# Kernel optimization log

Hardware: AMD Instinct MI355X
Metric: run time of the kernel (lower is better)

Reference implementation:

```python
import jax
import jax.numpy as jnp
from jax import lax
import numpy as np

IN_SCALE, IN_ZP = 0.01, 7
W_SCALE, W_ZP = 0.01, 3
B_SCALE = 0.0001
I32_MIN, I32_MAX = -(2.0**31), 2.0**31 - 1


def setup_inputs() -> dict:
    key = jax.random.key(0)
    k1, k2, k3 = jax.random.split(key, 3)
    # int8 quantized input activations and weights (torch passes torch.int8 tensors)
    inputVec = jax.random.randint(k1, (32, 128, 56, 56), -128, 128, dtype=jnp.int32).astype(jnp.int8)
    weight = jax.random.randint(k2, (256, 128, 3, 3), -128, 128, dtype=jnp.int32).astype(jnp.int8)
    bias = jax.random.normal(k3, (256,), dtype=jnp.float32)
    return {"inputVec": inputVec, "weight": weight, "bias": bias}


def reference(inputVec, weight, bias):
    # dequantize per-tensor: (q - zero_point) * scale
    x = (inputVec.astype(jnp.float32) - IN_ZP) * IN_SCALE   # [N, Cin, H, W]
    w = (weight.astype(jnp.float32) - W_ZP) * W_SCALE       # [Cout, Cin, kh, kw]
    # quantize bias to qint32 (round-half-even, clamp to int32 range) then dequantize
    b = jnp.clip(jnp.round(bias / B_SCALE), I32_MIN, I32_MAX) * B_SCALE  # [Cout]
    # conv2d: stride 1, no padding, dilation 1, groups 1
    out = lax.conv_general_dilated(
        x, w,
        window_strides=(1, 1),
        padding='VALID',
        dimension_numbers=('NCHW', 'OIHW', 'NCHW'),
    )  # [N, Cout, H-2, W-2]
    return out + b[None, :, None, None]
```

## Files before the change

kernel.cpp:

```cpp
#include <hip/hip_runtime.h>
#include <hip/hip_bf16.h>


#define N_B   32
#define C_IN  128
#define H_IN  56
#define W_IN  56
#define C_OUT 256
#define H_OUT 54
#define W_OUT 54
#define K_TOT 1152
#define NPX   (N_B * H_OUT * W_OUT)
#define PXROW (H_OUT * W_OUT)

using i32x4  = __attribute__((ext_vector_type(4))) int;

static __device__ __forceinline__ int dot4(int a, int b, int c) {
#if __has_builtin(__builtin_amdgcn_sdot4)
  return __builtin_amdgcn_sdot4(a, b, c, false);
#else
  signed char a0 = (signed char)a, a1 = (signed char)(a >> 8),
              a2 = (signed char)(a >> 16), a3 = (signed char)(a >> 24);
  signed char b0 = (signed char)b, b1 = (signed char)(b >> 8),
              b2 = (signed char)(b >> 16), b3 = (signed char)(b >> 24);
  return c + a0 * b0 + a1 * b1 + a2 * b2 + a3 * b3;
#endif
}

static __device__ __forceinline__ int pack4(int4 v) {
  return (v.x & 255) | ((v.y & 255) << 8) | ((v.z & 255) << 16) | ((v.w & 255) << 24);
}

__device__ __forceinline__ void gload16(const void* g, void* l) {
  __builtin_amdgcn_global_load_lds(
      (const __attribute__((address_space(1))) void*)g,
      (__attribute__((address_space(3))) void*)l, 16, 0, 0);
}

__global__ void prep(const int* __restrict__ in, const int* __restrict__ wsrc,
                     const float* __restrict__ bias,
                     signed char* __restrict__ ip2, int* __restrict__ rs,
                     signed char* __restrict__ wq3, float* __restrict__ bconst) {
  const int bid = blockIdx.x, tid = threadIdx.x;
  __shared__ int t32[W_IN][132];
  __shared__ int rsum[W_IN];

  if (bid < 1792) {
    const int h = bid % 56, n = bid / 56;
    if (tid < W_IN) rsum[tid] = 0;
    int ci = tid >> 1, hf = tid & 1;
    const int* s = in + ((size_t)n * C_IN + ci) * (H_IN * W_IN) + h * W_IN + hf * 28;
#pragma unroll
    for (int k = 0; k < 7; ++k) {
      int4 v = *(const int4*)(s + k * 4);
      int wr = hf * 28 + k * 4;
      t32[wr + 0][ci] = v.x;
      t32[wr + 1][ci] = v.y;
      t32[wr + 2][ci] = v.z;
      t32[wr + 3][ci] = v.w;
    }
    __syncthreads();

    signed char* dst = ip2 + ((size_t)n * H_IN + h) * 8192;
    for (int u = tid; u < 448; u += 256) {
      int w = u % 56, c16 = u / 56;
      int4 q0 = *(const int4*)&t32[w][c16 * 16 + 0];
      int4 q1 = *(const int4*)&t32[w][c16 * 16 + 4];
      int4 q2 = *(const int4*)&t32[w][c16 * 16 + 8];
      int4 q3 = *(const int4*)&t32[w][c16 * 16 + 12];
      int b[4];
      b[0] = pack4(q0); b[1] = pack4(q1); b[2] = pack4(q2); b[3] = pack4(q3);
      int srow = 0;
      srow = dot4(b[0], 0x01010101, srow);
      srow = dot4(b[1], 0x01010101, srow);
      srow = dot4(b[2], 0x01010101, srow);
      srow = dot4(b[3], 0x01010101, srow);
      *(int4*)(dst + (size_t)c16 * 1024 + w * 16) = *(int4*)b;
      atomicAdd(&rsum[w], srow);
    }
    __syncthreads();
    if (tid < W_IN) rs[((size_t)n * H_IN + h) * W_IN + tid] = rsum[tid];
  } else {
    int* red = &t32[0][0];
    const int co = (bid - 1792) * 2 + (tid >> 7);
    const int ci = tid & 127;
    const int* wrow = wsrc + (size_t)co * K_TOT + (size_t)ci * 9;
    int s = 0;
    int kk = ci >> 5, hh = (ci >> 4) & 1, b = ci & 15;
    size_t base = (size_t)kk * 8192 + hh * 4096 + co * 16 + b;
#pragma unroll
    for (int t = 0; t < 9; ++t) {
      int v = wrow[t];
      s += v;
      wq3[(size_t)t * 32768 + base] = (signed char)v;
    }
    red[tid] = s;
    __syncthreads();
    for (int off = 64; off > 0; off >>= 1) {
      if (ci < off) red[tid] += red[tid + off];
      __syncthreads();
    }
    if (ci == 0) {
      int wsum = red[tid];
      float r = rintf(bias[co] / 0.0001f);
      r = fminf(fmaxf(r, -2147483648.0f), 2147483647.0f);
      bconst[co] = 1e-4f * (float)(-7 * wsum + 24192) + r * 0.0001f;
    }
  }
}

__device__ __forceinline__ int mklb(int pf, int pxl, int c16) {
  int j = pf * 16 + pxl;
  int jc = j > 107 ? 107 : j;
  int dy = (jc >= 54) ? 1 : 0;
  return c16 * 4096 + dy * 1024 + (jc - dy * 54) * 16;
}

__launch_bounds__(256, 4)
__global__ void conv_mfma(const signed char* __restrict__ ip2,
                          const signed char* __restrict__ wq3,
                          const int* __restrict__ rs,
                          const float* __restrict__ bconst,
                          float* __restrict__ out) {
  __shared__ signed char lds[32768];
  __shared__ float asf_lds[112];
  const int tid = threadIdx.x, w = tid >> 6, l = tid & 63;
  const int c16 = l >> 4, pxl = l & 15;

  const int b0 = blockIdx.x;
  const int wg = (b0 & 7) * 216 + (b0 >> 3);
  const int cq = wg & 1;
  const int nr = wg >> 1;
  const int n  = nr / 27;
  const int rp = nr - n * 27;
  const int y0 = rp * 2;

  const signed char* ipn = ip2 + ((size_t)n * H_IN + y0) * 8192;
  {
    const int r = tid >> 6;
    const int off = (tid & 63) * 16;
    const signed char* src = ipn + (size_t)r * 8192 + off;
#pragma unroll
    for (int i = 0; i < 8; ++i)
      gload16(src + (size_t)i * 1024, &lds[i * 4096 + tid * 16]);
  }

  if (tid < 108) {
    int dy = (tid >= 54) ? 1 : 0;
    int x  = tid - dy * 54;
    const int* rp_ = rs + ((size_t)n * H_IN + y0 + dy) * W_IN + x;
    int s = 0;
#pragma unroll
    for (int kh = 0; kh < 3; ++kh)
      s += rp_[kh * W_IN + 0] + rp_[kh * W_IN + 1] + rp_[kh * W_IN + 2];
    asf_lds[tid] = -3e-4f * (float)s;
  }

  const int lb0 = mklb(0, pxl, c16), lb1 = mklb(1, pxl, c16), lb2 = mklb(2, pxl, c16),
            lb3 = mklb(3, pxl, c16), lb4 = mklb(4, pxl, c16), lb5 = mklb(5, pxl, c16),
            lb6 = mklb(6, pxl, c16);

  const signed char* awq = wq3 + (size_t)c16 * 4096 +
                           (size_t)(cq * 128 + w * 32 + pxl) * 16;

  i32x4 a0_0 = {0,0,0,0}, a0_1 = {0,0,0,0}, a0_2 = {0,0,0,0}, a0_3 = {0,0,0,0},
        a0_4 = {0,0,0,0}, a0_5 = {0,0,0,0}, a0_6 = {0,0,0,0};
  i32x4 a1_0 = {0,0,0,0}, a1_1 = {0,0,0,0}, a1_2 = {0,0,0,0}, a1_3 = {0,0,0,0},
        a1_4 = {0,0,0,0}, a1_5 = {0,0,0,0}, a1_6 = {0,0,0,0};
  i32x4 wa0, wa1, wb0, wb1;
  i32x4 qa0, qa1, qa2, qa3;
  i32x4 qb0, qb1, qb2;

#define LDW(P, t)                                                              \
  P##0 = *(const i32x4*)(awq + (size_t)(t) * 16384);                           \
  P##1 = *(const i32x4*)(awq + (size_t)(t) * 16384 + 256);

#define DOFF(ks) (((ks) & 1) * 16384 + (((ks) >> 1) / 3) * 1024 +              \
                  (((ks) >> 1) % 3) * 16)

#define RDQA(dd)                                                               \
  qa0 = *(const i32x4*)(&lds[lb0 + (dd)]);                                     \
  qa1 = *(const i32x4*)(&lds[lb1 + (dd)]);                                     \
  qa2 = *(const i32x4*)(&lds[lb2 + (dd)]);                                     \
  qa3 = *(const i32x4*)(&lds[lb3 + (dd)]);

#define RDQB(dd)                                                               \
  qb0 = *(const i32x4*)(&lds[lb4 + (dd)]);                                     \
  qb1 = *(const i32x4*)(&lds[lb5 + (dd)]);                                     \
  qb2 = *(const i32x4*)(&lds[lb6 + (dd)]);

#define MFA(U)                                                                 \
  __builtin_amdgcn_s_setprio(1);                                               \
  a0_0 = __builtin_amdgcn_mfma_i32_16x16x64_i8(U##0, qa0, a0_0, 0, 0, 0);      \
  a1_0 = __builtin_amdgcn_mfma_i32_16x16x64_i8(U##1, qa0, a1_0, 0, 0, 0);      \
  a0_1 = __builtin_amdgcn_mfma_i32_16x16x64_i8(U##0, qa1, a0_1, 0, 0, 0);      \
  a1_1 = __builtin_amdgcn_mfma_i32_16x16x64_i8(U##1, qa1, a1_1, 0, 0, 0);      \
  a0_2 = __builtin_amdgcn_mfma_i32_16x16x64_i8(U##0, qa2, a0_2, 0, 0, 0);      \
  a1_2 = __builtin_amdgcn_mfma_i32_16x16x64_i8(U##1, qa2, a1_2, 0, 0, 0);      \
  a0_3 = __builtin_amdgcn_mfma_i32_16x16x64_i8(U##0, qa3, a0_3, 0, 0, 0);      \
  a1_3 = __builtin_amdgcn_mfma_i32_16x16x64_i8(U##1, qa3, a1_3, 0, 0, 0);      \
  __builtin_amdgcn_s_setprio(0);

#define MFB(U)                                                                 \
  __builtin_amdgcn_s_setprio(1);                                               \
  a0_4 = __builtin_amdgcn_mfma_i32_16x16x64_i8(U##0, qb0, a0_4, 0, 0, 0);      \
  a1_4 = __builtin_amdgcn_mfma_i32_16x16x64_i8(U##1, qb0, a1_4, 0, 0, 0);      \
  a0_5 = __builtin_amdgcn_mfma_i32_16x16x64_i8(U##0, qb1, a0_5, 0, 0, 0);      \
  a1_5 = __builtin_amdgcn_mfma_i32_16x16x64_i8(U##1, qb1, a1_5, 0, 0, 0);      \
  a0_6 = __builtin_amdgcn_mfma_i32_16x16x64_i8(U##0, qb2, a0_6, 0, 0, 0);      \
  a1_6 = __builtin_amdgcn_mfma_i32_16x16x64_i8(U##1, qb2, a1_6, 0, 0, 0);      \
  __builtin_amdgcn_s_setprio(0);

#define KSTEP(ks, U, L, DOLOAD)                                                \
  {                                                                            \
    if (DOLOAD) { LDW(L, (ks) + 1); }                                          \
    RDQB(DOFF(ks));                                                            \
    MFA(U);                                                                    \
    if ((ks) < 17) { RDQA(DOFF(((ks) + 1) % 18)); }                            \
    MFB(U);                                                                    \
  }

  LDW(wa, 0);
  __syncthreads();

  RDQA(DOFF(0));

  KSTEP(0,  wa, wb, 1)  KSTEP(1,  wb, wa, 1)  KSTEP(2,  wa, wb, 1)
  KSTEP(3,  wb, wa, 1)  KSTEP(4,  wa, wb, 1)  KSTEP(5,  wb, wa, 1)
  KSTEP(6,  wa, wb, 1)  KSTEP(7,  wb, wa, 1)  KSTEP(8,  wa, wb, 1)
  KSTEP(9,  wb, wa, 1)  KSTEP(10, wa, wb, 1)  KSTEP(11, wb, wa, 1)
  KSTEP(12, wa, wb, 1)  KSTEP(13, wb, wa, 1)  KSTEP(14, wa, wb, 1)
  KSTEP(15, wb, wa, 1)  KSTEP(16, wa, wb, 1)  KSTEP(17, wb, wa, 0)
#undef KSTEP
#undef MFA
#undef MFB
#undef RDQA
#undef RDQB
#undef DOFF
#undef LDW

  float* obase = out + ((size_t)n * C_OUT + cq * 128) * PXROW + y0 * W_OUT;
  const float asf0 = asf_lds[pxl];
  const float asf1 = asf_lds[16 + pxl];
  const float asf2 = asf_lds[32 + pxl];
  const float asf3 = asf_lds[48 + pxl];
  const float asf4 = asf_lds[64 + pxl];
  const float asf5 = asf_lds[80 + pxl];
  const int j6 = 96 + pxl;
  const float asf6 = (j6 < 108) ? asf_lds[j6] : 0.0f;
#pragma unroll
  for (int m = 0; m < 2; ++m) {
#pragma unroll
    for (int j = 0; j < 4; ++j) {
      int co = w * 32 + m * 16 + c16 * 4 + j;
      float bc = bconst[cq * 128 + co];
      float* o = obase + (size_t)co * PXROW;
      const i32x4& v0 = m ? a1_0 : a0_0;
      const i32x4& v1 = m ? a1_1 : a0_1;
      const i32x4& v2 = m ? a1_2 : a0_2;
      const i32x4& v3 = m ? a1_3 : a0_3;
      const i32x4& v4 = m ? a1_4 : a0_4;
      const i32x4& v5 = m ? a1_5 : a0_5;
      const i32x4& v6 = m ? a1_6 : a0_6;
      o[pxl]      = 1e-4f * (float)v0[j] + asf0 + bc;
      o[16 + pxl] = 1e-4f * (float)v1[j] + asf1 + bc;
      o[32 + pxl] = 1e-4f * (float)v2[j] + asf2 + bc;
      o[48 + pxl] = 1e-4f * (float)v3[j] + asf3 + bc;
      o[64 + pxl] = 1e-4f * (float)v4[j] + asf4 + bc;
      o[80 + pxl] = 1e-4f * (float)v5[j] + asf5 + bc;
      if (j6 < 108)
        o[j6] = 1e-4f * (float)v6[j] + asf6 + bc;
    }
  }
}

__global__ void conv_naive(const int* __restrict__ in, const int* __restrict__ w,
                           const float* __restrict__ bias, float* __restrict__ out) {
  size_t idx = (size_t)blockIdx.x * 256 + threadIdx.x;
  size_t total = (size_t)N_B * C_OUT * H_OUT * W_OUT;
  if (idx >= total) return;
  int x = idx % W_OUT; size_t t = idx / W_OUT;
  int y = t % H_OUT; t /= H_OUT;
  int co = t % C_OUT; int n = (int)(t / C_OUT);
  int acc = 0;
  for (int ci = 0; ci < C_IN; ++ci) {
    const int* ib = in + (((size_t)n * C_IN + ci) * H_IN + y) * W_IN + x;
    const int* wb = w + (((size_t)co * C_IN + ci) * 3) * 3;
    for (int kh = 0; kh < 3; ++kh)
      for (int kw = 0; kw < 3; ++kw)
        acc += (ib[kh * W_IN + kw] - 7) * (wb[kh * 3 + kw] - 3);
  }
  float r = rintf(bias[co] / 0.0001f);
  r = fminf(fmaxf(r, -2147483648.0f), 2147483647.0f);
  out[idx] = (float)acc * (0.01f * 0.01f) + r * 0.0001f;
}

extern "C" void kernel_launch(void* const* d_in, const int* in_sizes, int n_in,
                              void* d_out, int out_size, void* d_ws, size_t ws_size,
                              hipStream_t stream) {
  const int*   in   = (const int*)d_in[0];
  const int*   w    = (const int*)d_in[1];
  const float* bias = (const float*)d_in[2];
  float*       out  = (float*)d_out;

  const size_t WQ_OFF = 0;
  const size_t IP_OFF = 294912;
  const size_t RS_OFF = IP_OFF + 14680064;
  const size_t BC_OFF = RS_OFF + 401408;
  const size_t NEED   = BC_OFF + 1024;

  if (ws_size >= NEED) {
    char* ws = (char*)d_ws;
    signed char* wq3  = (signed char*)(ws + WQ_OFF);
    signed char* ip2  = (signed char*)(ws + IP_OFF);
    int*         rs   = (int*)(ws + RS_OFF);
    float*       bc   = (float*)(ws + BC_OFF);

    prep<<<1920, 256, 0, stream>>>(in, w, bias, ip2, rs, wq3, bc);
    conv_mfma<<<1728, 256, 0, stream>>>(ip2, wq3, rs, bc, out);
  } else {
    size_t total = (size_t)N_B * C_OUT * H_OUT * W_OUT;
    conv_naive<<<(total + 255) / 256, 256, 0, stream>>>(in, w, bias, out);
  }
}
```

Baseline: 50.00 us.

## Compute all 256 output channels per block to reuse staged input tile

Each workgroup now covers all 256 output channels instead of half, so every wave accumulates 4 channel tiles (64 channels) rather than 2. This halves the grid to 864 blocks, so the input row pair staged into LDS and the row-sum work are done once per spatial tile instead of twice. In exchange it doubles the accumulator and weight registers and lowers the launch bound to 2 blocks per CU, which reduces occupancy and may hurt latency hiding and load balance across CUs.

```diff
diff --git a/kernel.cpp b/kernel.cpp
--- a/kernel.cpp
+++ b/kernel.cpp
@@ -116,7 +116,7 @@
   return c16 * 4096 + dy * 1024 + (jc - dy * 54) * 16;
 }
 
-__launch_bounds__(256, 4)
+__launch_bounds__(256, 2)
 __global__ void conv_mfma(const signed char* __restrict__ ip2,
                           const signed char* __restrict__ wq3,
                           const int* __restrict__ rs,
@@ -128,11 +128,9 @@
   const int c16 = l >> 4, pxl = l & 15;
 
   const int b0 = blockIdx.x;
-  const int wg = (b0 & 7) * 216 + (b0 >> 3);
-  const int cq = wg & 1;
-  const int nr = wg >> 1;
-  const int n  = nr / 27;
-  const int rp = nr - n * 27;
+  const int wg = (b0 & 7) * 108 + (b0 >> 3);
+  const int n  = wg / 27;
+  const int rp = wg - n * 27;
   const int y0 = rp * 2;
 
   const signed char* ipn = ip2 + ((size_t)n * H_IN + y0) * 8192;
@@ -161,19 +159,25 @@
             lb6 = mklb(6, pxl, c16);
 
   const signed char* awq = wq3 + (size_t)c16 * 4096 +
-                           (size_t)(cq * 128 + w * 32 + pxl) * 16;
-
-  i32x4 a0_0 = {0,0,0,0}, a0_1 = {0,0,0,0}, a0_2 = {0,0,0,0}, a0_3 = {0,0,0,0},
-        a0_4 = {0,0,0,0}, a0_5 = {0,0,0,0}, a0_6 = {0,0,0,0};
-  i32x4 a1_0 = {0,0,0,0}, a1_1 = {0,0,0,0}, a1_2 = {0,0,0,0}, a1_3 = {0,0,0,0},
-        a1_4 = {0,0,0,0}, a1_5 = {0,0,0,0}, a1_6 = {0,0,0,0};
-  i32x4 wa0, wa1, wb0, wb1;
+                           (size_t)(w * 64 + pxl) * 16;
+
+  i32x4 c0_0={0,0,0,0},c0_1={0,0,0,0},c0_2={0,0,0,0},c0_3={0,0,0,0},
+        c0_4={0,0,0,0},c0_5={0,0,0,0},c0_6={0,0,0,0};
+  i32x4 c1_0={0,0,0,0},c1_1={0,0,0,0},c1_2={0,0,0,0},c1_3={0,0,0,0},
+        c1_4={0,0,0,0},c1_5={0,0,0,0},c1_6={0,0,0,0};
+  i32x4 c2_0={0,0,0,0},c2_1={0,0,0,0},c2_2={0,0,0,0},c2_3={0,0,0,0},
+        c2_4={0,0,0,0},c2_5={0,0,0,0},c2_6={0,0,0,0};
+  i32x4 c3_0={0,0,0,0},c3_1={0,0,0,0},c3_2={0,0,0,0},c3_3={0,0,0,0},
+        c3_4={0,0,0,0},c3_5={0,0,0,0},c3_6={0,0,0,0};
+  i32x4 wa0, wa1, wa2, wa3, wb0, wb1, wb2, wb3;
   i32x4 qa0, qa1, qa2, qa3;
   i32x4 qb0, qb1, qb2;
 
 #define LDW(P, t)                                                              \
   P##0 = *(const i32x4*)(awq + (size_t)(t) * 16384);                           \
-  P##1 = *(const i32x4*)(awq + (size_t)(t) * 16384 + 256);
+  P##1 = *(const i32x4*)(awq + (size_t)(t) * 16384 + 256);                     \
+  P##2 = *(const i32x4*)(awq + (size_t)(t) * 16384 + 512);                     \
+  P##3 = *(const i32x4*)(awq + (size_t)(t) * 16384 + 768);
 
 #define DOFF(ks) (((ks) & 1) * 16384 + (((ks) >> 1) / 3) * 1024 +              \
                   (((ks) >> 1) % 3) * 16)
@@ -191,24 +195,38 @@
 
 #define MFA(U)                                                                 \
   __builtin_amdgcn_s_setprio(1);                                               \
-  a0_0 = __builtin_amdgcn_mfma_i32_16x16x64_i8(U##0, qa0, a0_0, 0, 0, 0);      \
-  a1_0 = __builtin_amdgcn_mfma_i32_16x16x64_i8(U##1, qa0, a1_0, 0, 0, 0);      \
-  a0_1 = __builtin_amdgcn_mfma_i32_16x16x64_i8(U##0, qa1, a0_1, 0, 0, 0);      \
-  a1_1 = __builtin_amdgcn_mfma_i32_16x16x64_i8(U##1, qa1, a1_1, 0, 0, 0);      \
-  a0_2 = __builtin_amdgcn_mfma_i32_16x16x64_i8(U##0, qa2, a0_2, 0, 0, 0);      \
-  a1_2 = __builtin_amdgcn_mfma_i32_16x16x64_i8(U##1, qa2, a1_2, 0, 0, 0);      \
-  a0_3 = __builtin_amdgcn_mfma_i32_16x16x64_i8(U##0, qa3, a0_3, 0, 0, 0);      \
-  a1_3 = __builtin_amdgcn_mfma_i32_16x16x64_i8(U##1, qa3, a1_3, 0, 0, 0);      \
+  c0_0 = __builtin_amdgcn_mfma_i32_16x16x64_i8(U##0, qa0, c0_0, 0, 0, 0);      \
+  c1_0 = __builtin_amdgcn_mfma_i32_16x16x64_i8(U##1, qa0, c1_0, 0, 0, 0);      \
+  c2_0 = __builtin_amdgcn_mfma_i32_16x16x64_i8(U##2, qa0, c2_0, 0, 0, 0);      \
+  c3_0 = __builtin_amdgcn_mfma_i32_16x16x64_i8(U##3, qa0, c3_0, 0, 0, 0);      \
+  c0_1 = __builtin_amdgcn_mfma_i32_16x16x64_i8(U##0, qa1, c0_1, 0, 0, 0);      \
+  c1_1 = __builtin_amdgcn_mfma_i32_16x16x64_i8(U##1, qa1, c1_1, 0, 0, 0);      \
+  c2_1 = __builtin_amdgcn_mfma_i32_16x16x64_i8(U##2, qa1, c2_1, 0, 0, 0);      \
+  c3_1 = __builtin_amdgcn_mfma_i32_16x16x64_i8(U##3, qa1, c3_1, 0, 0, 0);      \
+  c0_2 = __builtin_amdgcn_mfma_i32_16x16x64_i8(U##0, qa2, c0_2, 0, 0, 0);      \
+  c1_2 = __builtin_amdgcn_mfma_i32_16x16x64_i8(U##1, qa2, c1_2, 0, 0, 0);      \
+  c2_2 = __builtin_amdgcn_mfma_i32_16x16x64_i8(U##2, qa2, c2_2, 0, 0, 0);      \
+  c3_2 = __builtin_amdgcn_mfma_i32_16x16x64_i8(U##3, qa2, c3_2, 0, 0, 0);      \
+  c0_3 = __builtin_amdgcn_mfma_i32_16x16x64_i8(U##0, qa3, c0_3, 0, 0, 0);      \
+  c1_3 = __builtin_amdgcn_mfma_i32_16x16x64_i8(U##1, qa3, c1_3, 0, 0, 0);      \
+  c2_3 = __builtin_amdgcn_mfma_i32_16x16x64_i8(U##2, qa3, c2_3, 0, 0, 0);      \
+  c3_3 = __builtin_amdgcn_mfma_i32_16x16x64_i8(U##3, qa3, c3_3, 0, 0, 0);      \
   __builtin_amdgcn_s_setprio(0);
 
 #define MFB(U)                                                                 \
   __builtin_amdgcn_s_setprio(1);                                               \
-  a0_4 = __builtin_amdgcn_mfma_i32_16x16x64_i8(U##0, qb0, a0_4, 0, 0, 0);      \
-  a1_4 = __builtin_amdgcn_mfma_i32_16x16x64_i8(U##1, qb0, a1_4, 0, 0, 0);      \
-  a0_5 = __builtin_amdgcn_mfma_i32_16x16x64_i8(U##0, qb1, a0_5, 0, 0, 0);      \
-  a1_5 = __builtin_amdgcn_mfma_i32_16x16x64_i8(U##1, qb1, a1_5, 0, 0, 0);      \
-  a0_6 = __builtin_amdgcn_mfma_i32_16x16x64_i8(U##0, qb2, a0_6, 0, 0, 0);      \
-  a1_6 = __builtin_amdgcn_mfma_i32_16x16x64_i8(U##1, qb2, a1_6, 0, 0, 0);      \
+  c0_4 = __builtin_amdgcn_mfma_i32_16x16x64_i8(U##0, qb0, c0_4, 0, 0, 0);      \
+  c1_4 = __builtin_amdgcn_mfma_i32_16x16x64_i8(U##1, qb0, c1_4, 0, 0, 0);      \
+  c2_4 = __builtin_amdgcn_mfma_i32_16x16x64_i8(U##2, qb0, c2_4, 0, 0, 0);      \
+  c3_4 = __builtin_amdgcn_mfma_i32_16x16x64_i8(U##3, qb0, c3_4, 0, 0, 0);      \
+  c0_5 = __builtin_amdgcn_mfma_i32_16x16x64_i8(U##0, qb1, c0_5, 0, 0, 0);      \
+  c1_5 = __builtin_amdgcn_mfma_i32_16x16x64_i8(U##1, qb1, c1_5, 0, 0, 0);      \
+  c2_5 = __builtin_amdgcn_mfma_i32_16x16x64_i8(U##2, qb1, c2_5, 0, 0, 0);      \
+  c3_5 = __builtin_amdgcn_mfma_i32_16x16x64_i8(U##3, qb1, c3_5, 0, 0, 0);      \
+  c0_6 = __builtin_amdgcn_mfma_i32_16x16x64_i8(U##0, qb2, c0_6, 0, 0, 0);      \
+  c1_6 = __builtin_amdgcn_mfma_i32_16x16x64_i8(U##1, qb2, c1_6, 0, 0, 0);      \
+  c2_6 = __builtin_amdgcn_mfma_i32_16x16x64_i8(U##2, qb2, c2_6, 0, 0, 0);      \
+  c3_6 = __builtin_amdgcn_mfma_i32_16x16x64_i8(U##3, qb2, c3_6, 0, 0, 0);      \
   __builtin_amdgcn_s_setprio(0);
 
 #define KSTEP(ks, U, L, DOLOAD)                                                \
@@ -239,7 +257,7 @@
 #undef DOFF
 #undef LDW
 
-  float* obase = out + ((size_t)n * C_OUT + cq * 128) * PXROW + y0 * W_OUT;
+  float* obase = out + (size_t)n * C_OUT * PXROW + y0 * W_OUT;
   const float asf0 = asf_lds[pxl];
   const float asf1 = asf_lds[16 + pxl];
   const float asf2 = asf_lds[32 + pxl];
@@ -248,30 +266,27 @@
   const float asf5 = asf_lds[80 + pxl];
   const int j6 = 96 + pxl;
   const float asf6 = (j6 < 108) ? asf_lds[j6] : 0.0f;
-#pragma unroll
-  for (int m = 0; m < 2; ++m) {
-#pragma unroll
-    for (int j = 0; j < 4; ++j) {
-      int co = w * 32 + m * 16 + c16 * 4 + j;
-      float bc = bconst[cq * 128 + co];
-      float* o = obase + (size_t)co * PXROW;
-      const i32x4& v0 = m ? a1_0 : a0_0;
-      const i32x4& v1 = m ? a1_1 : a0_1;
-      const i32x4& v2 = m ? a1_2 : a0_2;
-      const i32x4& v3 = m ? a1_3 : a0_3;
-      const i32x4& v4 = m ? a1_4 : a0_4;
-      const i32x4& v5 = m ? a1_5 : a0_5;
-      const i32x4& v6 = m ? a1_6 : a0_6;
-      o[pxl]      = 1e-4f * (float)v0[j] + asf0 + bc;
-      o[16 + pxl] = 1e-4f * (float)v1[j] + asf1 + bc;
-      o[32 + pxl] = 1e-4f * (float)v2[j] + asf2 + bc;
-      o[48 + pxl] = 1e-4f * (float)v3[j] + asf3 + bc;
-      o[64 + pxl] = 1e-4f * (float)v4[j] + asf4 + bc;
-      o[80 + pxl] = 1e-4f * (float)v5[j] + asf5 + bc;
-      if (j6 < 108)
-        o[j6] = 1e-4f * (float)v6[j] + asf6 + bc;
-    }
-  }
+
+#define STM(m, V0, V1, V2, V3, V4, V5, V6)                                     \
+  {                                                                            \
+    _Pragma("unroll") for (int j = 0; j < 4; ++j) {                            \
+      int co = w * 64 + (m) * 16 + c16 * 4 + j;                                \
+      float bc = bconst[co];                                                   \
+      float* o = obase + (size_t)co * PXROW;                                   \
+      o[pxl]      = 1e-4f * (float)V0[j] + asf0 + bc;                          \
+      o[16 + pxl] = 1e-4f * (float)V1[j] + asf1 + bc;                          \
+      o[32 + pxl] = 1e-4f * (float)V2[j] + asf2 + bc;                          \
+      o[48 + pxl] = 1e-4f * (float)V3[j] + asf3 + bc;                          \
+      o[64 + pxl] = 1e-4f * (float)V4[j] + asf4 + bc;                          \
+      o[80 + pxl] = 1e-4f * (float)V5[j] + asf5 + bc;                          \
+      if (j6 < 108) o[j6] = 1e-4f * (float)V6[j] + asf6 + bc;                  \
+    }                                                                          \
+  }
+  STM(0, c0_0, c0_1, c0_2, c0_3, c0_4, c0_5, c0_6)
+  STM(1, c1_0, c1_1, c1_2, c1_3, c1_4, c1_5, c1_6)
+  STM(2, c2_0, c2_1, c2_2, c2_3, c2_4, c2_5, c2_6)
+  STM(3, c3_0, c3_1, c3_2, c3_3, c3_4, c3_5, c3_6)
+#undef STM
 }
 
 __global__ void conv_naive(const int* __restrict__ in, const int* __restrict__ w,
@@ -317,7 +332,7 @@
     float*       bc   = (float*)(ws + BC_OFF);
 
     prep<<<1920, 256, 0, stream>>>(in, w, bias, ip2, rs, wq3, bc);
-    conv_mfma<<<1728, 256, 0, stream>>>(ip2, wq3, rs, bc, out);
+    conv_mfma<<<864, 256, 0, stream>>>(ip2, wq3, rs, bc, out);
   } else {
     size_t total = (size_t)N_B * C_OUT * H_OUT * W_OUT;
     conv_naive<<<(total + 255) / 256, 256, 0, stream>>>(in, w, bias, out);
```

Measured after the change: 53.11 us. 6.2% more time.
